# Kernel optimization log

Hardware: AMD Instinct MI355X
Metric: run time of the kernel (lower is better)

## Reference

```python
import jax, jax.numpy as jnp
from jax import lax
import numpy as np

N_NODES = 5000
N_EDGES = 80000
N_FEAT = 128
N_TPLT = 16
TPLT_NODES = 10
N_FW = 3         # Frank-Wolfe (conditional-gradient) outer iterations
SINK_ITERS = 10  # log-domain Sinkhorn inner iterations


def setup_inputs() -> dict:
    key = jax.random.key(0)
    k1, k2, k3, k4, k5 = jax.random.split(key, 5)
    x = jax.random.normal(k1, (N_NODES, N_FEAT), jnp.float32)
    src = jax.random.randint(k2, (N_EDGES,), 0, N_NODES, jnp.int32)
    dst = jax.random.randint(k3, (N_EDGES,), 0, N_NODES, jnp.int32)
    edge_index = jnp.stack([src, dst], axis=0)
    A0 = jax.random.uniform(k4, (N_TPLT, TPLT_NODES, TPLT_NODES), jnp.float32)
    tplt_adjacencies = 0.5 * (A0 + jnp.transpose(A0, (0, 2, 1)))  # symmetrized, as in template_initialisation
    tplt_features = jax.random.normal(k5, (N_TPLT, TPLT_NODES, N_FEAT), jnp.float32)
    q0 = jnp.zeros((N_TPLT, TPLT_NODES), jnp.float32)   # softmax(q0) -> uniform template node weights
    alpha0 = jnp.zeros((1,), jnp.float32)               # sigmoid(alpha0) -> alpha = 0.5
    return {"x": x, "edge_index": edge_index, "tplt_adjacencies": tplt_adjacencies,
            "tplt_features": tplt_features, "q0": q0, "alpha0": alpha0}


def _sinkhorn_log(G, logp, logq, reg):
    """Log-domain Sinkhorn solving min <G,T> + reg*KL(T | p q^T); returns T [N, m]."""
    def step(carry, _):
        f, g = carry
        f = reg * (logp - jax.scipy.special.logsumexp((g[None, :] - G) / reg, axis=1))
        g = reg * (logq - jax.scipy.special.logsumexp((f[:, None] - G) / reg, axis=0))
        return (f, g), None
    (f, g), _ = lax.scan(step, (jnp.zeros_like(logp), jnp.zeros_like(logq)), None, length=SINK_ITERS)
    return jnp.exp((f[:, None] + g[None, :] - G) / reg)


def _fgw_dist(A, x, p, C2, F2, q, alpha):
    """Fused Gromov-Wasserstein distance (square loss) between graph (A, x, p)
    and one template (C2, F2, q), solved by conditional gradient with Sinkhorn
    inner OT solves and exact quadratic line search."""
    # pairwise squared-euclidean feature cost M [N, m]
    M = jnp.sum(x * x, 1)[:, None] + jnp.sum(F2 * F2, 1)[None, :] - 2.0 * (x @ F2.T)
    # square-loss Gromov decomposition: L(C1,C2) (x) T = constC - 2 * C1 T C2
    constC = ((A * A) @ p)[:, None] + ((C2 * C2) @ q)[None, :]
    logp, logq = jnp.log(p), jnp.log(q)
    T0 = p[:, None] * q[None, :]

    def fw_step(T, _):
        ATC = A @ (T @ C2)                        # [N, m]
        tens = constC - 2.0 * ATC
        G = (1.0 - alpha) * M + 2.0 * alpha * tens  # linearized gradient
        reg = 0.05 * jnp.mean(jnp.abs(G)) + 1e-9
        Tn = _sinkhorn_log(G, logp, logq, reg)
        dT = Tn - T
        AdTC = A @ (dT @ C2)
        # cost(T + g*dT) = a g^2 + b g + c  (square-loss FGW)
        a = -2.0 * alpha * jnp.sum(AdTC * dT)
        b = (1.0 - alpha) * jnp.sum(M * dT) + alpha * (jnp.sum(constC * dT) - 4.0 * jnp.sum(ATC * dT))
        gamma = jnp.where(a > 0.0, jnp.clip(-b / (2.0 * a + 1e-16), 0.0, 1.0),
                          jnp.where(a + b < 0.0, 1.0, 0.0))
        return T + gamma * dT, None

    T, _ = lax.scan(fw_step, T0, None, length=N_FW)
    ATC = A @ (T @ C2)
    return (1.0 - alpha) * jnp.sum(M * T) + alpha * (jnp.sum(constC * T) - 2.0 * jnp.sum(ATC * T))


def reference(x, edge_index, tplt_adjacencies, tplt_features, q0, alpha0):
    N = x.shape[0]
    # dense adjacency from COO edge list (to_dense_adj equivalent)
    A = jnp.zeros((N, N), x.dtype).at[edge_index[0], edge_index[1]].set(1.0)
    p = jnp.full((N,), 1.0 / N, x.dtype)       # uniform graph node weights
    alpha = jax.nn.sigmoid(alpha0[0])          # trained FGW trade-off (multi_alpha=False)
    q = jax.nn.softmax(q0, axis=1)             # trained template node weights
    dists = jax.vmap(lambda C2, F2, qk: _fgw_dist(A, x, p, C2, F2, qk, alpha))(
        tplt_adjacencies, tplt_features, q)
    return dists  # [n_tplt] FGW-distance embedding of the graph
```

## Files before the change

kernel.cpp:

```cpp
#include <hip/hip_runtime.h>
#include <stdint.h>

typedef float    f32x4 __attribute__((ext_vector_type(4)));
typedef uint32_t u32x4 __attribute__((ext_vector_type(4)));

#define NN 5000
#define NE 80000
#define NF 128
#define NT 16
#define TN 10
#define NFW 3
#define NSK 10
#define PW (1.0f/5000.0f)
#define RB 128
#define GRX 40

#define OFF_DEG  0u
#define OFF_RP   20224u
#define OFF_CUR  40448u
#define OFF_COL  60672u
#define OFF_SC   380672u
#define SC_FLOATS 384
#define OFF_M    393216u
#define OFF_T    4233216u
#define OFF_G    8073216u
#define OFF_ATCM 11913216u
#define OFF_ATCT 13193216u
#define OFF_ADTM 13513216u
#define OFF_ADTT 14793216u
#define OFF_TNM  15113216u
#define OFF_TNT  16393216u
#define OFF_Y2M  16713216u
#define OFF_Y2T  17993216u

__device__ __forceinline__ uint32_t bfb(float x) {
  uint32_t u = __float_as_uint(x);
  return (u + 0x7fffu + ((u >> 16) & 1u)) >> 16;
}
__device__ __forceinline__ uint32_t pk(float a, float b) { return bfb(a) | (bfb(b) << 16); }
__device__ __forceinline__ float ubl(uint32_t u) { return __uint_as_float(u << 16); }
__device__ __forceinline__ float ubh(uint32_t u) { return __uint_as_float(u & 0xffff0000u); }
__device__ __forceinline__ float sigm(float z) { return 1.f / (1.f + __expf(-z)); }

__device__ __forceinline__ void ld12(const float* p, float* v) {
  f32x4 a = *(const f32x4*)p, b = *(const f32x4*)(p + 4), c = *(const f32x4*)(p + 8);
  v[0]=a[0]; v[1]=a[1]; v[2]=a[2]; v[3]=a[3]; v[4]=b[0]; v[5]=b[1]; v[6]=b[2]; v[7]=b[3];
  v[8]=c[0]; v[9]=c[1];
}
__device__ __forceinline__ void st12(float* p, const float* v) {
  *(f32x4*)p       = (f32x4){v[0], v[1], v[2], v[3]};
  *(f32x4*)(p + 4) = (f32x4){v[4], v[5], v[6], v[7]};
  *(f32x4*)(p + 8) = (f32x4){v[8], v[9], 0.f, 0.f};
}
__device__ __forceinline__ void ldbf(const u32x4* __restrict__ M4, const uint32_t* __restrict__ M1,
                                     size_t i, float* v) {
  u32x4 A = M4[i]; uint32_t B = M1[i];
  v[0]=ubl(A[0]); v[1]=ubh(A[0]); v[2]=ubl(A[1]); v[3]=ubh(A[1]);
  v[4]=ubl(A[2]); v[5]=ubh(A[2]); v[6]=ubl(A[3]); v[7]=ubh(A[3]);
  v[8]=ubl(B);    v[9]=ubh(B);
}
__device__ __forceinline__ void stbf(u32x4* __restrict__ M4, uint32_t* __restrict__ M1,
                                     size_t i, const float* v) {
  M4[i] = (u32x4){pk(v[0], v[1]), pk(v[2], v[3]), pk(v[4], v[5]), pk(v[6], v[7])};
  M1[i] = pk(v[8], v[9]);
}

__device__ __forceinline__ void gath(const u32x4* __restrict__ YM, const uint32_t* __restrict__ YT,
                                     const int* __restrict__ col, int e0, int e1, float* acc) {
  for (int e = e0; e < e1; ++e) {
    int c = col[e];
    u32x4 A = YM[c]; uint32_t B = YT[c];
    acc[0] += ubl(A[0]); acc[1] += ubh(A[0]); acc[2] += ubl(A[1]); acc[3] += ubh(A[1]);
    acc[4] += ubl(A[2]); acc[5] += ubh(A[2]); acc[6] += ubl(A[3]); acc[7] += ubh(A[3]);
    acc[8] += ubl(B);    acc[9] += ubh(B);
  }
}

__device__ __forceinline__ float get_gamma(const float* __restrict__ sc, int t, int k,
                                           float alpha, float oma) {
  const float* dk = sc + 64 + (size_t)((t - 1) * NT + k) * 4;
  float a_ = -2.f * alpha * dk[3];
  float b_ = oma * dk[0] + alpha * (dk[1] - 4.f * dk[2]);
  return (a_ > 0.f) ? fminf(fmaxf(-b_ / (2.f * a_ + 1e-16f), 0.f), 1.f)
                    : ((a_ + b_ < 0.f) ? 1.f : 0.f);
}

__global__ void k_init(char* __restrict__ ws) {
  int g = blockIdx.x * 256 + threadIdx.x;
  if (g < NN) ((int*)(ws + OFF_DEG))[g] = 0;
  int z = g - NN;
  if (z >= 0 && z < SC_FLOATS) ((float*)(ws + OFF_SC))[z] = 0.f;
}
__global__ void k_deg(const int* __restrict__ ei, int* __restrict__ deg) {
  int e = blockIdx.x * 256 + threadIdx.x;
  if (e < NE) atomicAdd(&deg[ei[e]], 1);
}
__global__ void k_scan(const int* __restrict__ deg, int* __restrict__ rowptr, int* __restrict__ cur) {
  __shared__ int scr[1024];
  int tid = threadIdx.x;
  int loc[5], s = 0;
  #pragma unroll
  for (int r = 0; r < 5; ++r) {
    int idx = tid * 5 + r;
    int d = (idx < NN) ? deg[idx] : 0;
    loc[r] = s; s += d;
  }
  scr[tid] = s; __syncthreads();
  for (int off = 1; off < 1024; off <<= 1) {
    int v = scr[tid];
    int u = (tid >= off) ? scr[tid - off] : 0;
    __syncthreads();
    scr[tid] = v + u;
    __syncthreads();
  }
  int base = (tid > 0) ? scr[tid - 1] : 0;
  #pragma unroll
  for (int r = 0; r < 5; ++r) {
    int idx = tid * 5 + r;
    if (idx < NN) { int v = base + loc[r]; rowptr[idx] = v; cur[idx] = v; }
  }
  if (tid == 1023) rowptr[NN] = scr[1023];
}
__global__ void k_fill(const int* __restrict__ ei, int* __restrict__ cur, int* __restrict__ col) {
  int e = blockIdx.x * 256 + threadIdx.x;
  if (e < NE) {
    int s = ei[e];
    int pos = atomicAdd(&cur[s], 1);
    col[pos] = ei[NE + e];
  }
}

__global__ void kM(const float* __restrict__ x, const float* __restrict__ F2,
                   float* __restrict__ Mb) {
  __shared__ float ffs[TN];
  const int k = blockIdx.y, tid = threadIdx.x;
  const int i = blockIdx.x * RB + tid;
  const float* Fk = F2 + (size_t)k * TN * NF;
  if (tid < TN) {
    float s = 0.f;
    for (int d = 0; d < NF; ++d) { float f = Fk[tid * NF + d]; s += f * f; }
    ffs[tid] = s;
  }
  __syncthreads();
  if (i >= NN) return;
  const f32x4* xr = (const f32x4*)(x + (size_t)i * NF);
  float acc[TN];
  #pragma unroll
  for (int j = 0; j < TN; ++j) acc[j] = 0.f;
  float xsq = 0.f;
  for (int dc = 0; dc < NF / 4; ++dc) {
    f32x4 xv = xr[dc];
    xsq += xv[0]*xv[0] + xv[1]*xv[1] + xv[2]*xv[2] + xv[3]*xv[3];
    #pragma unroll
    for (int j = 0; j < TN; ++j) {
      const float* Fj = Fk + j * NF + dc * 4;
      acc[j] += xv[0]*Fj[0] + xv[1]*Fj[1] + xv[2]*Fj[2] + xv[3]*Fj[3];
    }
  }
  float v[TN];
  #pragma unroll
  for (int j = 0; j < TN; ++j) v[j] = xsq + ffs[j] - 2.f * acc[j];
  st12(Mb + ((size_t)k * NN + i) * 12, v);
}

__global__ void kYG(const int* __restrict__ rowptr, const float* __restrict__ Mb,
                    float* __restrict__ Tb,
                    const u32x4* __restrict__ TnM, const uint32_t* __restrict__ TnT,
                    u32x4* __restrict__ AtM, uint32_t* __restrict__ AtT,
                    const u32x4* __restrict__ AdM, const uint32_t* __restrict__ AdT_,
                    float* __restrict__ Gb, const float* __restrict__ q0,
                    const float* __restrict__ C2g, const float* __restrict__ a0,
                    float* __restrict__ sc, int t) {
  __shared__ float qvs[16], c2qs[16], qC2s[16];
  __shared__ float redl[2];
  const int k = blockIdx.y, tid = threadIdx.x;
  const int i = blockIdx.x * RB + tid;
  const float* C2k = C2g + k * 100;
  if (tid < TN) {
    float mx = -1e30f, e[TN], s = 0.f;
    #pragma unroll
    for (int j = 0; j < TN; ++j) mx = fmaxf(mx, q0[k * TN + j]);
    #pragma unroll
    for (int j = 0; j < TN; ++j) { e[j] = __expf(q0[k * TN + j] - mx); s += e[j]; }
    float inv = 1.f / s;
    qvs[tid] = e[tid] * inv;
    float c2 = 0.f, qc = 0.f;
    #pragma unroll
    for (int l = 0; l < TN; ++l) {
      float c = C2k[tid * TN + l];
      c2 += c * c * e[l] * inv;
      qc += e[l] * inv * C2k[l * TN + tid];
    }
    c2qs[tid] = c2; qC2s[tid] = qc;
  }
  __syncthreads();
  const float alpha = sigm(a0[0]), oma = 1.f - alpha;
  float sabs = 0.f;
  if (i < NN) {
    const int deg = rowptr[i + 1] - rowptr[i];
    const float cc = (float)deg * PW;
    const size_t ro = ((size_t)k * NN + i) * 12;
    const size_t bi = (size_t)k * NN + i;
    float Trow[TN], Arow[TN];
    if (t == 0) {
      #pragma unroll
      for (int j = 0; j < TN; ++j) { Trow[j] = PW * qvs[j]; Arow[j] = (float)deg * PW * qC2s[j]; }
    } else {
      const float gamma = get_gamma(sc, t, k, alpha, oma);
      float tv[TN], nv[TN], av[TN], dv[TN];
      ld12(Tb + ro, tv);
      ldbf(TnM, TnT, bi, nv);
      ldbf(AtM, AtT, bi, av);
      ldbf(AdM, AdT_, bi, dv);
      #pragma unroll
      for (int j = 0; j < TN; ++j) {
        Trow[j] = tv[j] + gamma * (nv[j] - tv[j]);
        Arow[j] = av[j] + gamma * dv[j];
      }
    }
    st12(Tb + ro, Trow);
    stbf(AtM, AtT, bi, Arow);
    float mv[TN]; ld12(Mb + ro, mv);
    float Gv[TN];
    #pragma unroll
    for (int j = 0; j < TN; ++j) {
      float G = oma * mv[j] + 2.f * alpha * (cc + c2qs[j] - 2.f * Arow[j]);
      Gv[j] = G; sabs += fabsf(G);
    }
    st12(Gb + ro, Gv);
  }
  #pragma unroll
  for (int o = 32; o; o >>= 1) sabs += __shfl_xor(sabs, o, 64);
  if ((tid & 63) == 0) redl[tid >> 6] = sabs;
  __syncthreads();
  if (tid == 0) atomicAdd(sc + t * NT + k, redl[0] + redl[1]);
}

__global__ __launch_bounds__(1024) void kSink(const float* __restrict__ Gb,
                                              u32x4* __restrict__ TnM, uint32_t* __restrict__ TnT,
                                              const float* __restrict__ q0,
                                              const float* __restrict__ sc, int t) {
  __shared__ float red[16 * 16];
  __shared__ float wls[16];
  const int k = blockIdx.x, tid = threadIdx.x;
  const int wid = tid >> 6;
  float qme = 0.f;
  if (tid < TN) {
    float mx = -1e30f, e[TN], s = 0.f;
    #pragma unroll
    for (int j = 0; j < TN; ++j) mx = fmaxf(mx, q0[k * TN + j]);
    #pragma unroll
    for (int j = 0; j < TN; ++j) { e[j] = __expf(q0[k * TN + j] - mx); s += e[j]; }
    qme = e[tid] / s;
  }
  const float reg = 0.05f * sc[t * NT + k] * (1.f / (float)(NN * TN)) + 1e-9f;
  const float invreg = 1.f / reg;
  const float* Gk = Gb + (size_t)k * NN * 12;

  float E[5][TN];
  bool v[5];
  #pragma unroll
  for (int s = 0; s < 5; ++s) {
    int i = s * 1024 + tid;
    v[s] = i < NN;
    if (v[s]) ld12(Gk + (size_t)i * 12, E[s]);
  }
  #pragma unroll
  for (int s = 0; s < 5; ++s) {
    if (v[s]) {
      float mn = E[s][0];
      #pragma unroll
      for (int j = 1; j < TN; ++j) mn = fminf(mn, E[s][j]);
      #pragma unroll
      for (int j = 0; j < TN; ++j) E[s][j] = __expf(-(E[s][j] - mn) * invreg);
    } else {
      #pragma unroll
      for (int j = 0; j < TN; ++j) E[s][j] = 0.f;
    }
  }

  float wlr[TN], wpr[TN];
  #pragma unroll
  for (int j = 0; j < TN; ++j) { wlr[j] = 1.f; wpr[j] = 1.f; }
  for (int it = 0; it < NSK; ++it) {
    float csl[TN];
    #pragma unroll
    for (int j = 0; j < TN; ++j) csl[j] = 0.f;
    #pragma unroll
    for (int s = 0; s < 5; ++s) {
      float dot = 0.f;
      #pragma unroll
      for (int j = 0; j < TN; ++j) dot += E[s][j] * wlr[j];
      float u = PW * __builtin_amdgcn_rcpf(fmaxf(dot, 1e-35f));
      #pragma unroll
      for (int j = 0; j < TN; ++j) csl[j] += E[s][j] * u;
    }
    #pragma unroll
    for (int j = 0; j < TN; ++j) {
      float vv = csl[j];
      #pragma unroll
      for (int o = 32; o; o >>= 1) vv += __shfl_xor(vv, o, 64);
      if ((tid & 63) == j) red[wid * 16 + j] = vv;
    }
    __syncthreads();
    if (tid < TN) {
      float s = 0.f;
      #pragma unroll
      for (int w = 0; w < 16; ++w) s += red[w * 16 + tid];
      wls[tid] = qme * __builtin_amdgcn_rcpf(fmaxf(s, 1e-35f));
    }
    __syncthreads();
    #pragma unroll
    for (int j = 0; j < TN; ++j) { wpr[j] = wlr[j]; wlr[j] = wls[j]; }
  }
  u32x4* TM = TnM + (size_t)k * NN;
  uint32_t* TT = TnT + (size_t)k * NN;
  #pragma unroll
  for (int s = 0; s < 5; ++s) {
    if (v[s]) {
      int i = s * 1024 + tid;
      float dot = 0.f;
      #pragma unroll
      for (int j = 0; j < TN; ++j) dot += E[s][j] * wpr[j];
      float u = PW * __builtin_amdgcn_rcpf(fmaxf(dot, 1e-35f));
      float tn[TN];
      #pragma unroll
      for (int j = 0; j < TN; ++j) tn[j] = u * E[s][j] * wlr[j];
      stbf(TM, TT, (size_t)i, tn);
    }
  }
}

__global__ void kDT(const int* __restrict__ rowptr, const float* __restrict__ Mb,
                    const float* __restrict__ Tb,
                    const u32x4* __restrict__ TnM, const uint32_t* __restrict__ TnT,
                    const float* __restrict__ q0, const float* __restrict__ C2g,
                    u32x4* __restrict__ Y2M, uint32_t* __restrict__ Y2T,
                    float* __restrict__ sc, int t) {
  __shared__ float c2qs[16];
  __shared__ float redl[4];
  const int k = blockIdx.y, tid = threadIdx.x;
  const int i = blockIdx.x * RB + tid;
  const float* C2k = C2g + k * 100;
  if (tid < TN) {
    float mx = -1e30f, e[TN], s = 0.f;
    #pragma unroll
    for (int j = 0; j < TN; ++j) mx = fmaxf(mx, q0[k * TN + j]);
    #pragma unroll
    for (int j = 0; j < TN; ++j) { e[j] = __expf(q0[k * TN + j] - mx); s += e[j]; }
    float inv = 1.f / s, c2 = 0.f;
    #pragma unroll
    for (int l = 0; l < TN; ++l) { float c = C2k[tid * TN + l]; c2 += c * c * e[l] * inv; }
    c2qs[tid] = c2;
  }
  __syncthreads();
  float bM = 0.f, bC = 0.f;
  if (i < NN) {
    const size_t ro = ((size_t)k * NN + i) * 12;
    const size_t bi = (size_t)k * NN + i;
    float tv[TN], nv[TN], mv[TN], d[TN];
    ld12(Tb + ro, tv); ldbf(TnM, TnT, bi, nv); ld12(Mb + ro, mv);
    float cc = (float)(rowptr[i + 1] - rowptr[i]) * PW;
    #pragma unroll
    for (int j = 0; j < TN; ++j) {
      d[j] = nv[j] - tv[j];
      bM += mv[j] * d[j];
      bC += (cc + c2qs[j]) * d[j];
    }
    float y[TN];
    #pragma unroll
    for (int j = 0; j < TN; ++j) {
      float s = 0.f;
      #pragma unroll
      for (int l = 0; l < TN; ++l) s += d[l] * C2k[l * TN + j];
      y[j] = s;
    }
    stbf(Y2M + (size_t)k * NN, Y2T + (size_t)k * NN, (size_t)i, y);
  }
  #pragma unroll
  for (int o = 32; o; o >>= 1) { bM += __shfl_xor(bM, o, 64); bC += __shfl_xor(bC, o, 64); }
  if ((tid & 63) == 0) { int w = tid >> 6; redl[w * 2] = bM; redl[w * 2 + 1] = bC; }
  __syncthreads();
  if (tid == 0) {
    float* dk = sc + 64 + (size_t)(t * NT + k) * 4;
    atomicAdd(dk + 0, redl[0] + redl[2]);
    atomicAdd(dk + 1, redl[1] + redl[3]);
  }
}

__global__ void kA(const int* __restrict__ rowptr, const int* __restrict__ col,
                   const float* __restrict__ Tb,
                   const u32x4* __restrict__ TnM, const uint32_t* __restrict__ TnT,
                   const u32x4* __restrict__ AtM, const uint32_t* __restrict__ AtT,
                   const u32x4* __restrict__ Y2M, const uint32_t* __restrict__ Y2T,
                   u32x4* __restrict__ AdM, uint32_t* __restrict__ AdT_,
                   float* __restrict__ sc, int t) {
  __shared__ float redl[4];
  const int k = blockIdx.y, tid = threadIdx.x;
  const int i = blockIdx.x * RB + tid;
  float bA = 0.f, aacc = 0.f;
  if (i < NN) {
    const size_t ro = ((size_t)k * NN + i) * 12;
    const size_t bi = (size_t)k * NN + i;
    float tv[TN], nv[TN], av[TN];
    ld12(Tb + ro, tv); ldbf(TnM, TnT, bi, nv); ldbf(AtM, AtT, bi, av);
    int e0 = rowptr[i], e1 = rowptr[i + 1];
    float adt[TN];
    #pragma unroll
    for (int j = 0; j < TN; ++j) adt[j] = 0.f;
    gath(Y2M + (size_t)k * NN, Y2T + (size_t)k * NN, col, e0, e1, adt);
    #pragma unroll
    for (int j = 0; j < TN; ++j) {
      float d = nv[j] - tv[j];
      bA += av[j] * d;
      aacc += adt[j] * d;
    }
    stbf(AdM, AdT_, bi, adt);
  }
  #pragma unroll
  for (int o = 32; o; o >>= 1) { bA += __shfl_xor(bA, o, 64); aacc += __shfl_xor(aacc, o, 64); }
  if ((tid & 63) == 0) { int w = tid >> 6; redl[w * 2] = bA; redl[w * 2 + 1] = aacc; }
  __syncthreads();
  if (tid == 0) {
    float* dk = sc + 64 + (size_t)(t * NT + k) * 4;
    atomicAdd(dk + 2, redl[0] + redl[2]);
    atomicAdd(dk + 3, redl[1] + redl[3]);
  }
}

__global__ void kFinYG(const int* __restrict__ rowptr, const float* __restrict__ Mb,
                       const float* __restrict__ Tb,
                       const u32x4* __restrict__ TnM, const uint32_t* __restrict__ TnT,
                       const u32x4* __restrict__ AtM, const uint32_t* __restrict__ AtT,
                       const u32x4* __restrict__ AdM, const uint32_t* __restrict__ AdT_,
                       const float* __restrict__ q0, const float* __restrict__ C2g,
                       const float* __restrict__ a0, float* __restrict__ sc,
                       float* __restrict__ out) {
  __shared__ float c2qs[16];
  __shared__ float redl[6];
  const int k = blockIdx.y, tid = threadIdx.x;
  const int i = blockIdx.x * RB + tid;
  const float* C2k = C2g + k * 100;
  if (tid < TN) {
    float mx = -1e30f, e[TN], s = 0.f;
    #pragma unroll
    for (int j = 0; j < TN; ++j) mx = fmaxf(mx, q0[k * TN + j]);
    #pragma unroll
    for (int j = 0; j < TN; ++j) { e[j] = __expf(q0[k * TN + j] - mx); s += e[j]; }
    float inv = 1.f / s, c2 = 0.f;
    #pragma unroll
    for (int l = 0; l < TN; ++l) { float c = C2k[tid * TN + l]; c2 += c * c * e[l] * inv; }
    c2qs[tid] = c2;
  }
  __syncthreads();
  const float alpha = sigm(a0[0]), oma = 1.f - alpha;
  const float gamma = get_gamma(sc, NFW, k, alpha, oma);
  float d1 = 0.f, d2 = 0.f, d3 = 0.f;
  if (i < NN) {
    const size_t ro = ((size_t)k * NN + i) * 12;
    const size_t bi = (size_t)k * NN + i;
    float tv[TN], nv[TN], av[TN], dv[TN], mv[TN];
    ld12(Tb + ro, tv); ldbf(TnM, TnT, bi, nv);
    ldbf(AtM, AtT, bi, av); ldbf(AdM, AdT_, bi, dv);
    ld12(Mb + ro, mv);
    float cc = (float)(rowptr[i + 1] - rowptr[i]) * PW;
    #pragma unroll
    for (int j = 0; j < TN; ++j) {
      float Tf = tv[j] + gamma * (nv[j] - tv[j]);
      float Af = av[j] + gamma * dv[j];
      d1 += mv[j] * Tf;
      d2 += (cc + c2qs[j]) * Tf;
      d3 += Af * Tf;
    }
  }
  #pragma unroll
  for (int o = 32; o; o >>= 1) {
    d1 += __shfl_xor(d1, o, 64); d2 += __shfl_xor(d2, o, 64); d3 += __shfl_xor(d3, o, 64);
  }
  if ((tid & 63) == 0) {
    int w = tid >> 6;
    redl[w * 3] = d1; redl[w * 3 + 1] = d2; redl[w * 3 + 2] = d3;
  }
  __syncthreads();
  float* fk = sc + 256 + k * 4;
  if (tid == 0) {
    atomicAdd(fk + 0, redl[0] + redl[3]);
    atomicAdd(fk + 1, redl[1] + redl[4]);
    atomicAdd(fk + 2, redl[2] + redl[5]);
  }
  asm volatile("s_waitcnt vmcnt(0)" ::: "memory");
  __syncthreads();
  if (tid == 0) {
    int* ctr = (int*)sc + 320 + k;
    int old = __hip_atomic_fetch_add(ctr, 1, __ATOMIC_RELAXED, __HIP_MEMORY_SCOPE_AGENT);
    if (old == GRX - 1) {
      float f0 = __hip_atomic_fetch_add(fk + 0, 0.f, __ATOMIC_RELAXED, __HIP_MEMORY_SCOPE_AGENT);
      float f1 = __hip_atomic_fetch_add(fk + 1, 0.f, __ATOMIC_RELAXED, __HIP_MEMORY_SCOPE_AGENT);
      float f2 = __hip_atomic_fetch_add(fk + 2, 0.f, __ATOMIC_RELAXED, __HIP_MEMORY_SCOPE_AGENT);
      out[k] = oma * f0 + alpha * (f1 - 2.f * f2);
    }
  }
}

extern "C" void kernel_launch(void* const* d_in, const int* in_sizes, int n_in,
                              void* d_out, int out_size, void* d_ws, size_t ws_size,
                              hipStream_t stream) {
  const float* x  = (const float*)d_in[0];
  const int*   ei = (const int*)d_in[1];
  const float* C2 = (const float*)d_in[2];
  const float* F2 = (const float*)d_in[3];
  const float* q0 = (const float*)d_in[4];
  const float* a0 = (const float*)d_in[5];
  float* out = (float*)d_out;

  char* ws = (char*)d_ws;
  int* deg    = (int*)(ws + OFF_DEG);
  int* rowptr = (int*)(ws + OFF_RP);
  int* cur    = (int*)(ws + OFF_CUR);
  int* col    = (int*)(ws + OFF_COL);
  float* sc   = (float*)(ws + OFF_SC);
  float* Mb   = (float*)(ws + OFF_M);
  float* Tb   = (float*)(ws + OFF_T);
  float* Gb   = (float*)(ws + OFF_G);
  u32x4* AtM  = (u32x4*)(ws + OFF_ATCM);
  uint32_t* AtT = (uint32_t*)(ws + OFF_ATCT);
  u32x4* AdM  = (u32x4*)(ws + OFF_ADTM);
  uint32_t* AdT_ = (uint32_t*)(ws + OFF_ADTT);
  u32x4* TnM  = (u32x4*)(ws + OFF_TNM);
  uint32_t* TnT = (uint32_t*)(ws + OFF_TNT);
  u32x4* Y2M  = (u32x4*)(ws + OFF_Y2M);
  uint32_t* Y2T = (uint32_t*)(ws + OFF_Y2T);

  const dim3 rg(GRX, NT), rb(RB);

  k_init<<<(NN + SC_FLOATS + 255) / 256, 256, 0, stream>>>(ws);
  k_deg<<<(NE + 255) / 256, 256, 0, stream>>>(ei, deg);
  k_scan<<<1, 1024, 0, stream>>>(deg, rowptr, cur);
  k_fill<<<(NE + 255) / 256, 256, 0, stream>>>(ei, cur, col);
  kM<<<rg, rb, 0, stream>>>(x, F2, Mb);

  for (int t = 0; t < NFW; ++t) {
    kYG<<<rg, rb, 0, stream>>>(rowptr, Mb, Tb, TnM, TnT, AtM, AtT, AdM, AdT_,
                               Gb, q0, C2, a0, sc, t);
    kSink<<<NT, 1024, 0, stream>>>(Gb, TnM, TnT, q0, sc, t);
    kDT<<<rg, rb, 0, stream>>>(rowptr, Mb, Tb, TnM, TnT, q0, C2, Y2M, Y2T, sc, t);
    kA<<<rg, rb, 0, stream>>>(rowptr, col, Tb, TnM, TnT, AtM, AtT, Y2M, Y2T,
                              AdM, AdT_, sc, t);
  }
  kFinYG<<<rg, rb, 0, stream>>>(rowptr, Mb, Tb, TnM, TnT, AtM, AtT, AdM, AdT_,
                                q0, C2, a0, sc, out);
}
```

Before: 436.9 us.

## Fuse FW iteration kernels into cooperative per-template kernel with group barriers

Replaces the four per-iteration kernels (gradient, Sinkhorn, direction, adjacency product) with one cooperative kernel per Frank-Wolfe step. Each template is handled by 16 blocks that keep their rows' T, A·T·C2, cost and Gibbs kernel in registers, and Sinkhorn column sums are exchanged through global atomics and spin barriers. The line-search update is folded into the start of the next launch, so the G buffer and the Tn buffer are no longer written or read. This cuts kernel launch count and round-trips through global memory. In exchange it adds ten spin barriers per iteration over global atomics, and its correctness depends on all 256 blocks being co-resident.

```diff
diff --git a/kernel.cpp b/kernel.cpp
--- a/kernel.cpp
+++ b/kernel.cpp
@@ -14,24 +14,26 @@
 #define PW (1.0f/5000.0f)
 #define RB 128
 #define GRX 40
+#define NBT 16
+#define TPB 320
+#define RPB 313
 
 #define OFF_DEG  0u
 #define OFF_RP   20224u
 #define OFF_CUR  40448u
 #define OFF_COL  60672u
 #define OFF_SC   380672u
+#define OFF_CS   382208u
+#define OFF_M    416000u
+#define OFF_T    4256000u
+#define OFF_ATM  8096000u
+#define OFF_ATT  9376000u
+#define OFF_DTM  9696000u
+#define OFF_DTT  10976000u
+#define OFF_Y2M  11296000u
+#define OFF_Y2T  12576000u
 #define SC_FLOATS 384
-#define OFF_M    393216u
-#define OFF_T    4233216u
-#define OFF_G    8073216u
-#define OFF_ATCM 11913216u
-#define OFF_ATCT 13193216u
-#define OFF_ADTM 13513216u
-#define OFF_ADTT 14793216u
-#define OFF_TNM  15113216u
-#define OFF_TNT  16393216u
-#define OFF_Y2M  16713216u
-#define OFF_Y2T  17993216u
+#define CS_FLOATS 7680
 
 __device__ __forceinline__ uint32_t bfb(float x) {
   uint32_t u = __float_as_uint(x);
@@ -64,7 +66,6 @@
   M4[i] = (u32x4){pk(v[0], v[1]), pk(v[2], v[3]), pk(v[4], v[5]), pk(v[6], v[7])};
   M1[i] = pk(v[8], v[9]);
 }
-
 __device__ __forceinline__ void gath(const u32x4* __restrict__ YM, const uint32_t* __restrict__ YT,
                                      const int* __restrict__ col, int e0, int e1, float* acc) {
   for (int e = e0; e < e1; ++e) {
@@ -75,14 +76,26 @@
     acc[8] += ubl(B);    acc[9] += ubh(B);
   }
 }
-
-__device__ __forceinline__ float get_gamma(const float* __restrict__ sc, int t, int k,
-                                           float alpha, float oma) {
-  const float* dk = sc + 64 + (size_t)((t - 1) * NT + k) * 4;
-  float a_ = -2.f * alpha * dk[3];
-  float b_ = oma * dk[0] + alpha * (dk[1] - 4.f * dk[2]);
-  return (a_ > 0.f) ? fminf(fmaxf(-b_ / (2.f * a_ + 1e-16f), 0.f), 1.f)
-                    : ((a_ + b_ < 0.f) ? 1.f : 0.f);
+__device__ __forceinline__ float ga_readf(float* p) {
+  return __hip_atomic_fetch_add(p, 0.0f, __ATOMIC_RELAXED, __HIP_MEMORY_SCOPE_AGENT);
+}
+__device__ __forceinline__ void tbar(int* ctr, int target) {
+  asm volatile("s_waitcnt vmcnt(0)" ::: "memory");
+  __syncthreads();
+  if (threadIdx.x == 0) {
+    __hip_atomic_fetch_add(ctr, 1, __ATOMIC_RELAXED, __HIP_MEMORY_SCOPE_AGENT);
+    while (__hip_atomic_fetch_add(ctr, 0, __ATOMIC_RELAXED, __HIP_MEMORY_SCOPE_AGENT) < target)
+      __builtin_amdgcn_s_sleep(8);
+  }
+  __syncthreads();
+}
+__device__ __forceinline__ float bred(float v, float* red) {
+  #pragma unroll
+  for (int o = 32; o; o >>= 1) v += __shfl_xor(v, o, 64);
+  __syncthreads();
+  if ((threadIdx.x & 63) == 0) red[threadIdx.x >> 6] = v;
+  __syncthreads();
+  return red[0] + red[1] + red[2] + red[3] + red[4];
 }
 
 __global__ void k_init(char* __restrict__ ws) {
@@ -90,6 +103,8 @@
   if (g < NN) ((int*)(ws + OFF_DEG))[g] = 0;
   int z = g - NN;
   if (z >= 0 && z < SC_FLOATS) ((float*)(ws + OFF_SC))[z] = 0.f;
+  int c = g - (NN + SC_FLOATS);
+  if (c >= 0 && c < CS_FLOATS) ((float*)(ws + OFF_CS))[c] = 0.f;
 }
 __global__ void k_deg(const int* __restrict__ ei, int* __restrict__ deg) {
   int e = blockIdx.x * 256 + threadIdx.x;
@@ -129,7 +144,6 @@
     col[pos] = ei[NE + e];
   }
 }
-
 __global__ void kM(const float* __restrict__ x, const float* __restrict__ F2,
                    float* __restrict__ Mb) {
   __shared__ float ffs[TN];
@@ -163,18 +177,21 @@
   st12(Mb + ((size_t)k * NN + i) * 12, v);
 }
 
-__global__ void kYG(const int* __restrict__ rowptr, const float* __restrict__ Mb,
-                    float* __restrict__ Tb,
-                    const u32x4* __restrict__ TnM, const uint32_t* __restrict__ TnT,
-                    u32x4* __restrict__ AtM, uint32_t* __restrict__ AtT,
-                    const u32x4* __restrict__ AdM, const uint32_t* __restrict__ AdT_,
-                    float* __restrict__ Gb, const float* __restrict__ q0,
-                    const float* __restrict__ C2g, const float* __restrict__ a0,
-                    float* __restrict__ sc, int t) {
+__global__ __launch_bounds__(TPB, 2) void kFW(
+    const int* __restrict__ rowptr, const int* __restrict__ col,
+    const float* __restrict__ Mb, float* __restrict__ Tb,
+    u32x4* __restrict__ AtM, uint32_t* __restrict__ AtT,
+    u32x4* __restrict__ DtM, uint32_t* __restrict__ DtT,
+    u32x4* __restrict__ Y2M, uint32_t* __restrict__ Y2T,
+    const float* __restrict__ q0, const float* __restrict__ C2g,
+    const float* __restrict__ a0p, float* __restrict__ sc,
+    float* __restrict__ csg, int t) {
+  __shared__ float red[80];
+  __shared__ float csb[16];
   __shared__ float qvs[16], c2qs[16], qC2s[16];
-  __shared__ float redl[2];
-  const int k = blockIdx.y, tid = threadIdx.x;
-  const int i = blockIdx.x * RB + tid;
+  const int bid = blockIdx.x;
+  const int k = bid >> 4, b = bid & (NBT - 1);
+  const int tid = threadIdx.x;
   const float* C2k = C2g + k * 100;
   if (tid < TN) {
     float mx = -1e30f, e[TN], s = 0.f;
@@ -194,153 +211,157 @@
     c2qs[tid] = c2; qC2s[tid] = qc;
   }
   __syncthreads();
-  const float alpha = sigm(a0[0]), oma = 1.f - alpha;
+  const float alpha = sigm(a0p[0]), oma = 1.f - alpha;
+  int* ctr = (int*)sc + 320 + t * 16 + k;
+  int barno = 0;
+
+  const int r = b * RPB + tid;
+  const bool own = (tid < RPB) && (r < NN);
+  int e0 = 0, e1 = 0;
+  if (own) { e0 = rowptr[r]; e1 = rowptr[r + 1]; }
+  const float cc = (float)(e1 - e0) * PW;
+  const size_t bi = (size_t)k * NN + (own ? r : 0);
+
+  float Tr[TN], Ar[TN];
+  if (t == 0) {
+    if (own) {
+      #pragma unroll
+      for (int j = 0; j < TN; ++j) { Tr[j] = PW * qvs[j]; Ar[j] = (float)(e1 - e0) * PW * qC2s[j]; }
+    }
+  } else {
+    float adt[TN] = {0,0,0,0,0,0,0,0,0,0};
+    float av[TN], dv[TN];
+    float bA = 0.f, aA = 0.f;
+    if (own) {
+      gath(Y2M + (size_t)k * NN, Y2T + (size_t)k * NN, col, e0, e1, adt);
+      ldbf(AtM, AtT, bi, av); ldbf(DtM, DtT, bi, dv);
+      #pragma unroll
+      for (int j = 0; j < TN; ++j) { bA += av[j] * dv[j]; aA += adt[j] * dv[j]; }
+    }
+    bA = bred(bA, red); aA = bred(aA, red);
+    float* dk = sc + 64 + (size_t)((t - 1) * NT + k) * 4;
+    if (tid == 0) { atomicAdd(dk + 2, bA); atomicAdd(dk + 3, aA); }
+    tbar(ctr, ++barno * NBT);
+    if (tid < 4) csb[tid] = ga_readf(dk + tid);
+    __syncthreads();
+    float a_ = -2.f * alpha * csb[3];
+    float b_ = oma * csb[0] + alpha * (csb[1] - 4.f * csb[2]);
+    float gamma = (a_ > 0.f) ? fminf(fmaxf(-b_ / (2.f * a_ + 1e-16f), 0.f), 1.f)
+                             : ((a_ + b_ < 0.f) ? 1.f : 0.f);
+    if (own) {
+      float tv[TN]; ld12(Tb + bi * 12, tv);
+      #pragma unroll
+      for (int j = 0; j < TN; ++j) { Tr[j] = tv[j] + gamma * dv[j]; Ar[j] = av[j] + gamma * adt[j]; }
+    }
+  }
+  float Mr[TN], Er[TN];
   float sabs = 0.f;
-  if (i < NN) {
-    const int deg = rowptr[i + 1] - rowptr[i];
-    const float cc = (float)deg * PW;
-    const size_t ro = ((size_t)k * NN + i) * 12;
-    const size_t bi = (size_t)k * NN + i;
-    float Trow[TN], Arow[TN];
-    if (t == 0) {
-      #pragma unroll
-      for (int j = 0; j < TN; ++j) { Trow[j] = PW * qvs[j]; Arow[j] = (float)deg * PW * qC2s[j]; }
-    } else {
-      const float gamma = get_gamma(sc, t, k, alpha, oma);
-      float tv[TN], nv[TN], av[TN], dv[TN];
-      ld12(Tb + ro, tv);
-      ldbf(TnM, TnT, bi, nv);
-      ldbf(AtM, AtT, bi, av);
-      ldbf(AdM, AdT_, bi, dv);
-      #pragma unroll
-      for (int j = 0; j < TN; ++j) {
-        Trow[j] = tv[j] + gamma * (nv[j] - tv[j]);
-        Arow[j] = av[j] + gamma * dv[j];
-      }
-    }
-    st12(Tb + ro, Trow);
-    stbf(AtM, AtT, bi, Arow);
-    float mv[TN]; ld12(Mb + ro, mv);
-    float Gv[TN];
-    #pragma unroll
-    for (int j = 0; j < TN; ++j) {
-      float G = oma * mv[j] + 2.f * alpha * (cc + c2qs[j] - 2.f * Arow[j]);
-      Gv[j] = G; sabs += fabsf(G);
-    }
-    st12(Gb + ro, Gv);
-  }
-  #pragma unroll
-  for (int o = 32; o; o >>= 1) sabs += __shfl_xor(sabs, o, 64);
-  if ((tid & 63) == 0) redl[tid >> 6] = sabs;
-  __syncthreads();
-  if (tid == 0) atomicAdd(sc + t * NT + k, redl[0] + redl[1]);
-}
-
-__global__ __launch_bounds__(1024) void kSink(const float* __restrict__ Gb,
-                                              u32x4* __restrict__ TnM, uint32_t* __restrict__ TnT,
-                                              const float* __restrict__ q0,
-                                              const float* __restrict__ sc, int t) {
-  __shared__ float red[16 * 16];
-  __shared__ float wls[16];
-  const int k = blockIdx.x, tid = threadIdx.x;
-  const int wid = tid >> 6;
-  float qme = 0.f;
-  if (tid < TN) {
-    float mx = -1e30f, e[TN], s = 0.f;
-    #pragma unroll
-    for (int j = 0; j < TN; ++j) mx = fmaxf(mx, q0[k * TN + j]);
-    #pragma unroll
-    for (int j = 0; j < TN; ++j) { e[j] = __expf(q0[k * TN + j] - mx); s += e[j]; }
-    qme = e[tid] / s;
-  }
-  const float reg = 0.05f * sc[t * NT + k] * (1.f / (float)(NN * TN)) + 1e-9f;
-  const float invreg = 1.f / reg;
-  const float* Gk = Gb + (size_t)k * NN * 12;
-
-  float E[5][TN];
-  bool v[5];
-  #pragma unroll
-  for (int s = 0; s < 5; ++s) {
-    int i = s * 1024 + tid;
-    v[s] = i < NN;
-    if (v[s]) ld12(Gk + (size_t)i * 12, E[s]);
-  }
-  #pragma unroll
-  for (int s = 0; s < 5; ++s) {
-    if (v[s]) {
-      float mn = E[s][0];
-      #pragma unroll
-      for (int j = 1; j < TN; ++j) mn = fminf(mn, E[s][j]);
-      #pragma unroll
-      for (int j = 0; j < TN; ++j) E[s][j] = __expf(-(E[s][j] - mn) * invreg);
-    } else {
-      #pragma unroll
-      for (int j = 0; j < TN; ++j) E[s][j] = 0.f;
-    }
+  if (own) {
+    st12(Tb + bi * 12, Tr);
+    stbf(AtM, AtT, bi, Ar);
+    ld12(Mb + bi * 12, Mr);
+    #pragma unroll
+    for (int j = 0; j < TN; ++j) {
+      float G = oma * Mr[j] + 2.f * alpha * (cc + c2qs[j] - 2.f * Ar[j]);
+      Er[j] = G; sabs += fabsf(G);
+    }
+  }
+  sabs = bred(sabs, red);
+  if (tid == 0) atomicAdd(sc + t * NT + k, sabs);
+  tbar(ctr, ++barno * NBT);
+  if (tid == 0) csb[0] = ga_readf(sc + t * NT + k);
+  __syncthreads();
+  const float invreg = 1.f / (0.05f * csb[0] * (1.f / (float)(NN * TN)) + 1e-9f);
+  if (own) {
+    float mn = Er[0];
+    #pragma unroll
+    for (int j = 1; j < TN; ++j) mn = fminf(mn, Er[j]);
+    #pragma unroll
+    for (int j = 0; j < TN; ++j) Er[j] = __expf(-(Er[j] - mn) * invreg);
+  } else {
+    #pragma unroll
+    for (int j = 0; j < TN; ++j) Er[j] = 0.f;
   }
 
   float wlr[TN], wpr[TN];
   #pragma unroll
   for (int j = 0; j < TN; ++j) { wlr[j] = 1.f; wpr[j] = 1.f; }
   for (int it = 0; it < NSK; ++it) {
+    float dot = 0.f;
+    #pragma unroll
+    for (int j = 0; j < TN; ++j) dot += Er[j] * wlr[j];
+    float u = PW * __builtin_amdgcn_rcpf(fmaxf(dot, 1e-35f));
     float csl[TN];
     #pragma unroll
-    for (int j = 0; j < TN; ++j) csl[j] = 0.f;
-    #pragma unroll
-    for (int s = 0; s < 5; ++s) {
-      float dot = 0.f;
-      #pragma unroll
-      for (int j = 0; j < TN; ++j) dot += E[s][j] * wlr[j];
-      float u = PW * __builtin_amdgcn_rcpf(fmaxf(dot, 1e-35f));
-      #pragma unroll
-      for (int j = 0; j < TN; ++j) csl[j] += E[s][j] * u;
-    }
+    for (int j = 0; j < TN; ++j) csl[j] = Er[j] * u;
     #pragma unroll
     for (int j = 0; j < TN; ++j) {
       float vv = csl[j];
       #pragma unroll
       for (int o = 32; o; o >>= 1) vv += __shfl_xor(vv, o, 64);
-      if ((tid & 63) == j) red[wid * 16 + j] = vv;
+      if ((tid & 63) == j) red[(tid >> 6) * 16 + j] = vv;
     }
     __syncthreads();
+    float* cell = csg + (size_t)((t * NSK + it) * NT + k) * 16;
     if (tid < TN) {
+      float s = red[tid] + red[16 + tid] + red[32 + tid] + red[48 + tid] + red[64 + tid];
+      atomicAdd(cell + tid, s);
+    }
+    tbar(ctr, ++barno * NBT);
+    if (tid < TN) csb[tid] = ga_readf(cell + tid);
+    __syncthreads();
+    #pragma unroll
+    for (int j = 0; j < TN; ++j) {
+      wpr[j] = wlr[j];
+      wlr[j] = qvs[j] * __builtin_amdgcn_rcpf(fmaxf(csb[j], 1e-35f));
+    }
+  }
+
+  float bM = 0.f, bC = 0.f;
+  if (own) {
+    float dot = 0.f;
+    #pragma unroll
+    for (int j = 0; j < TN; ++j) dot += Er[j] * wpr[j];
+    float u = PW * __builtin_amdgcn_rcpf(fmaxf(dot, 1e-35f));
+    float dT[TN];
+    #pragma unroll
+    for (int j = 0; j < TN; ++j) {
+      float tn = u * Er[j] * wlr[j];
+      dT[j] = tn - Tr[j];
+      bM += Mr[j] * dT[j];
+      bC += (cc + c2qs[j]) * dT[j];
+    }
+    stbf(DtM, DtT, bi, dT);
+    float y[TN];
+    #pragma unroll
+    for (int j = 0; j < TN; ++j) {
       float s = 0.f;
       #pragma unroll
-      for (int w = 0; w < 16; ++w) s += red[w * 16 + tid];
-      wls[tid] = qme * __builtin_amdgcn_rcpf(fmaxf(s, 1e-35f));
-    }
-    __syncthreads();
-    #pragma unroll
-    for (int j = 0; j < TN; ++j) { wpr[j] = wlr[j]; wlr[j] = wls[j]; }
-  }
-  u32x4* TM = TnM + (size_t)k * NN;
-  uint32_t* TT = TnT + (size_t)k * NN;
-  #pragma unroll
-  for (int s = 0; s < 5; ++s) {
-    if (v[s]) {
-      int i = s * 1024 + tid;
-      float dot = 0.f;
-      #pragma unroll
-      for (int j = 0; j < TN; ++j) dot += E[s][j] * wpr[j];
-      float u = PW * __builtin_amdgcn_rcpf(fmaxf(dot, 1e-35f));
-      float tn[TN];
-      #pragma unroll
-      for (int j = 0; j < TN; ++j) tn[j] = u * E[s][j] * wlr[j];
-      stbf(TM, TT, (size_t)i, tn);
-    }
-  }
-}
-
-__global__ void kDT(const int* __restrict__ rowptr, const float* __restrict__ Mb,
-                    const float* __restrict__ Tb,
-                    const u32x4* __restrict__ TnM, const uint32_t* __restrict__ TnT,
-                    const float* __restrict__ q0, const float* __restrict__ C2g,
-                    u32x4* __restrict__ Y2M, uint32_t* __restrict__ Y2T,
-                    float* __restrict__ sc, int t) {
+      for (int l = 0; l < TN; ++l) s += dT[l] * C2k[l * TN + j];
+      y[j] = s;
+    }
+    stbf(Y2M, Y2T, bi, y);
+  }
+  bM = bred(bM, red); bC = bred(bC, red);
+  float* dk2 = sc + 64 + (size_t)(t * NT + k) * 4;
+  if (tid == 0) { atomicAdd(dk2 + 0, bM); atomicAdd(dk2 + 1, bC); }
+}
+
+__global__ __launch_bounds__(TPB, 2) void kFin(
+    const int* __restrict__ rowptr, const int* __restrict__ col,
+    const float* __restrict__ Mb, const float* __restrict__ Tb,
+    const u32x4* __restrict__ AtM, const uint32_t* __restrict__ AtT,
+    const u32x4* __restrict__ DtM, const uint32_t* __restrict__ DtT,
+    const u32x4* __restrict__ Y2M, const uint32_t* __restrict__ Y2T,
+    const float* __restrict__ q0, const float* __restrict__ C2g,
+    const float* __restrict__ a0p, float* __restrict__ sc,
+    float* __restrict__ out) {
+  __shared__ float red[80];
+  __shared__ float csb[16];
   __shared__ float c2qs[16];
-  __shared__ float redl[4];
-  const int k = blockIdx.y, tid = threadIdx.x;
-  const int i = blockIdx.x * RB + tid;
+  const int bid = blockIdx.x;
+  const int k = bid >> 4, b = bid & (NBT - 1);
+  const int tid = threadIdx.x;
   const float* C2k = C2g + k * 100;
   if (tid < TN) {
     float mx = -1e30f, e[TN], s = 0.f;
@@ -354,152 +375,53 @@
     c2qs[tid] = c2;
   }
   __syncthreads();
-  float bM = 0.f, bC = 0.f;
-  if (i < NN) {
-    const size_t ro = ((size_t)k * NN + i) * 12;
-    const size_t bi = (size_t)k * NN + i;
-    float tv[TN], nv[TN], mv[TN], d[TN];
-    ld12(Tb + ro, tv); ldbf(TnM, TnT, bi, nv); ld12(Mb + ro, mv);
-    float cc = (float)(rowptr[i + 1] - rowptr[i]) * PW;
-    #pragma unroll
-    for (int j = 0; j < TN; ++j) {
-      d[j] = nv[j] - tv[j];
-      bM += mv[j] * d[j];
-      bC += (cc + c2qs[j]) * d[j];
-    }
-    float y[TN];
-    #pragma unroll
-    for (int j = 0; j < TN; ++j) {
-      float s = 0.f;
-      #pragma unroll
-      for (int l = 0; l < TN; ++l) s += d[l] * C2k[l * TN + j];
-      y[j] = s;
-    }
-    stbf(Y2M + (size_t)k * NN, Y2T + (size_t)k * NN, (size_t)i, y);
-  }
-  #pragma unroll
-  for (int o = 32; o; o >>= 1) { bM += __shfl_xor(bM, o, 64); bC += __shfl_xor(bC, o, 64); }
-  if ((tid & 63) == 0) { int w = tid >> 6; redl[w * 2] = bM; redl[w * 2 + 1] = bC; }
-  __syncthreads();
-  if (tid == 0) {
-    float* dk = sc + 64 + (size_t)(t * NT + k) * 4;
-    atomicAdd(dk + 0, redl[0] + redl[2]);
-    atomicAdd(dk + 1, redl[1] + redl[3]);
-  }
-}
-
-__global__ void kA(const int* __restrict__ rowptr, const int* __restrict__ col,
-                   const float* __restrict__ Tb,
-                   const u32x4* __restrict__ TnM, const uint32_t* __restrict__ TnT,
-                   const u32x4* __restrict__ AtM, const uint32_t* __restrict__ AtT,
-                   const u32x4* __restrict__ Y2M, const uint32_t* __restrict__ Y2T,
-                   u32x4* __restrict__ AdM, uint32_t* __restrict__ AdT_,
-                   float* __restrict__ sc, int t) {
-  __shared__ float redl[4];
-  const int k = blockIdx.y, tid = threadIdx.x;
-  const int i = blockIdx.x * RB + tid;
-  float bA = 0.f, aacc = 0.f;
-  if (i < NN) {
-    const size_t ro = ((size_t)k * NN + i) * 12;
-    const size_t bi = (size_t)k * NN + i;
-    float tv[TN], nv[TN], av[TN];
-    ld12(Tb + ro, tv); ldbf(TnM, TnT, bi, nv); ldbf(AtM, AtT, bi, av);
-    int e0 = rowptr[i], e1 = rowptr[i + 1];
-    float adt[TN];
-    #pragma unroll
-    for (int j = 0; j < TN; ++j) adt[j] = 0.f;
+  const float alpha = sigm(a0p[0]), oma = 1.f - alpha;
+  int* ctr = (int*)sc + 320 + 3 * 16 + k;
+  const int r = b * RPB + tid;
+  const bool own = (tid < RPB) && (r < NN);
+  int e0 = 0, e1 = 0;
+  if (own) { e0 = rowptr[r]; e1 = rowptr[r + 1]; }
+  const float cc = (float)(e1 - e0) * PW;
+  const size_t bi = (size_t)k * NN + (own ? r : 0);
+
+  float adt[TN] = {0,0,0,0,0,0,0,0,0,0};
+  float av[TN], dv[TN];
+  float bA = 0.f, aA = 0.f;
+  if (own) {
     gath(Y2M + (size_t)k * NN, Y2T + (size_t)k * NN, col, e0, e1, adt);
-    #pragma unroll
-    for (int j = 0; j < TN; ++j) {
-      float d = nv[j] - tv[j];
-      bA += av[j] * d;
-      aacc += adt[j] * d;
-    }
-    stbf(AdM, AdT_, bi, adt);
-  }
-  #pragma unroll
-  for (int o = 32; o; o >>= 1) { bA += __shfl_xor(bA, o, 64); aacc += __shfl_xor(aacc, o, 64); }
-  if ((tid & 63) == 0) { int w = tid >> 6; redl[w * 2] = bA; redl[w * 2 + 1] = aacc; }
-  __syncthreads();
-  if (tid == 0) {
-    float* dk = sc + 64 + (size_t)(t * NT + k) * 4;
-    atomicAdd(dk + 2, redl[0] + redl[2]);
-    atomicAdd(dk + 3, redl[1] + redl[3]);
-  }
-}
-
-__global__ void kFinYG(const int* __restrict__ rowptr, const float* __restrict__ Mb,
-                       const float* __restrict__ Tb,
-                       const u32x4* __restrict__ TnM, const uint32_t* __restrict__ TnT,
-                       const u32x4* __restrict__ AtM, const uint32_t* __restrict__ AtT,
-                       const u32x4* __restrict__ AdM, const uint32_t* __restrict__ AdT_,
-                       const float* __restrict__ q0, const float* __restrict__ C2g,
-                       const float* __restrict__ a0, float* __restrict__ sc,
-                       float* __restrict__ out) {
-  __shared__ float c2qs[16];
-  __shared__ float redl[6];
-  const int k = blockIdx.y, tid = threadIdx.x;
-  const int i = blockIdx.x * RB + tid;
-  const float* C2k = C2g + k * 100;
-  if (tid < TN) {
-    float mx = -1e30f, e[TN], s = 0.f;
-    #pragma unroll
-    for (int j = 0; j < TN; ++j) mx = fmaxf(mx, q0[k * TN + j]);
-    #pragma unroll
-    for (int j = 0; j < TN; ++j) { e[j] = __expf(q0[k * TN + j] - mx); s += e[j]; }
-    float inv = 1.f / s, c2 = 0.f;
-    #pragma unroll
-    for (int l = 0; l < TN; ++l) { float c = C2k[tid * TN + l]; c2 += c * c * e[l] * inv; }
-    c2qs[tid] = c2;
-  }
-  __syncthreads();
-  const float alpha = sigm(a0[0]), oma = 1.f - alpha;
-  const float gamma = get_gamma(sc, NFW, k, alpha, oma);
+    ldbf(AtM, AtT, bi, av); ldbf(DtM, DtT, bi, dv);
+    #pragma unroll
+    for (int j = 0; j < TN; ++j) { bA += av[j] * dv[j]; aA += adt[j] * dv[j]; }
+  }
+  bA = bred(bA, red); aA = bred(aA, red);
+  float* dk = sc + 64 + (size_t)((NFW - 1) * NT + k) * 4;
+  if (tid == 0) { atomicAdd(dk + 2, bA); atomicAdd(dk + 3, aA); }
+  tbar(ctr, 1 * NBT);
+  if (tid < 4) csb[tid] = ga_readf(dk + tid);
+  __syncthreads();
+  float a_ = -2.f * alpha * csb[3];
+  float b_ = oma * csb[0] + alpha * (csb[1] - 4.f * csb[2]);
+  float gamma = (a_ > 0.f) ? fminf(fmaxf(-b_ / (2.f * a_ + 1e-16f), 0.f), 1.f)
+                           : ((a_ + b_ < 0.f) ? 1.f : 0.f);
   float d1 = 0.f, d2 = 0.f, d3 = 0.f;
-  if (i < NN) {
-    const size_t ro = ((size_t)k * NN + i) * 12;
-    const size_t bi = (size_t)k * NN + i;
-    float tv[TN], nv[TN], av[TN], dv[TN], mv[TN];
-    ld12(Tb + ro, tv); ldbf(TnM, TnT, bi, nv);
-    ldbf(AtM, AtT, bi, av); ldbf(AdM, AdT_, bi, dv);
-    ld12(Mb + ro, mv);
-    float cc = (float)(rowptr[i + 1] - rowptr[i]) * PW;
-    #pragma unroll
-    for (int j = 0; j < TN; ++j) {
-      float Tf = tv[j] + gamma * (nv[j] - tv[j]);
-      float Af = av[j] + gamma * dv[j];
+  if (own) {
+    float tv[TN], mv[TN];
+    ld12(Tb + bi * 12, tv); ld12(Mb + bi * 12, mv);
+    #pragma unroll
+    for (int j = 0; j < TN; ++j) {
+      float Tf = tv[j] + gamma * dv[j];
+      float Af = av[j] + gamma * adt[j];
       d1 += mv[j] * Tf;
       d2 += (cc + c2qs[j]) * Tf;
       d3 += Af * Tf;
     }
   }
-  #pragma unroll
-  for (int o = 32; o; o >>= 1) {
-    d1 += __shfl_xor(d1, o, 64); d2 += __shfl_xor(d2, o, 64); d3 += __shfl_xor(d3, o, 64);
-  }
-  if ((tid & 63) == 0) {
-    int w = tid >> 6;
-    redl[w * 3] = d1; redl[w * 3 + 1] = d2; redl[w * 3 + 2] = d3;
-  }
-  __syncthreads();
+  d1 = bred(d1, red); d2 = bred(d2, red); d3 = bred(d3, red);
   float* fk = sc + 256 + k * 4;
-  if (tid == 0) {
-    atomicAdd(fk + 0, redl[0] + redl[3]);
-    atomicAdd(fk + 1, redl[1] + redl[4]);
-    atomicAdd(fk + 2, redl[2] + redl[5]);
-  }
-  asm volatile("s_waitcnt vmcnt(0)" ::: "memory");
-  __syncthreads();
-  if (tid == 0) {
-    int* ctr = (int*)sc + 320 + k;
-    int old = __hip_atomic_fetch_add(ctr, 1, __ATOMIC_RELAXED, __HIP_MEMORY_SCOPE_AGENT);
-    if (old == GRX - 1) {
-      float f0 = __hip_atomic_fetch_add(fk + 0, 0.f, __ATOMIC_RELAXED, __HIP_MEMORY_SCOPE_AGENT);
-      float f1 = __hip_atomic_fetch_add(fk + 1, 0.f, __ATOMIC_RELAXED, __HIP_MEMORY_SCOPE_AGENT);
-      float f2 = __hip_atomic_fetch_add(fk + 2, 0.f, __ATOMIC_RELAXED, __HIP_MEMORY_SCOPE_AGENT);
-      out[k] = oma * f0 + alpha * (f1 - 2.f * f2);
-    }
-  }
+  if (tid == 0) { atomicAdd(fk + 0, d1); atomicAdd(fk + 1, d2); atomicAdd(fk + 2, d3); }
+  tbar(ctr, 2 * NBT);
+  if (b == 0 && tid == 0)
+    out[k] = oma * ga_readf(fk + 0) + alpha * (ga_readf(fk + 1) - 2.f * ga_readf(fk + 2));
 }
 
 extern "C" void kernel_launch(void* const* d_in, const int* in_sizes, int n_in,
@@ -510,7 +432,7 @@
   const float* C2 = (const float*)d_in[2];
   const float* F2 = (const float*)d_in[3];
   const float* q0 = (const float*)d_in[4];
-  const float* a0 = (const float*)d_in[5];
+  const float* a0p = (const float*)d_in[5];
   float* out = (float*)d_out;
 
   char* ws = (char*)d_ws;
@@ -519,34 +441,36 @@
   int* cur    = (int*)(ws + OFF_CUR);
   int* col    = (int*)(ws + OFF_COL);
   float* sc   = (float*)(ws + OFF_SC);
+  float* csg  = (float*)(ws + OFF_CS);
   float* Mb   = (float*)(ws + OFF_M);
   float* Tb   = (float*)(ws + OFF_T);
-  float* Gb   = (float*)(ws + OFF_G);
-  u32x4* AtM  = (u32x4*)(ws + OFF_ATCM);
-  uint32_t* AtT = (uint32_t*)(ws + OFF_ATCT);
-  u32x4* AdM  = (u32x4*)(ws + OFF_ADTM);
-  uint32_t* AdT_ = (uint32_t*)(ws + OFF_ADTT);
-  u32x4* TnM  = (u32x4*)(ws + OFF_TNM);
-  uint32_t* TnT = (uint32_t*)(ws + OFF_TNT);
+  u32x4* AtM  = (u32x4*)(ws + OFF_ATM);
+  uint32_t* AtT = (uint32_t*)(ws + OFF_ATT);
+  u32x4* DtM  = (u32x4*)(ws + OFF_DTM);
+  uint32_t* DtT = (uint32_t*)(ws + OFF_DTT);
   u32x4* Y2M  = (u32x4*)(ws + OFF_Y2M);
   uint32_t* Y2T = (uint32_t*)(ws + OFF_Y2T);
 
-  const dim3 rg(GRX, NT), rb(RB);
-
-  k_init<<<(NN + SC_FLOATS + 255) / 256, 256, 0, stream>>>(ws);
+  int initN = NN + SC_FLOATS + CS_FLOATS;
+  k_init<<<(initN + 255) / 256, 256, 0, stream>>>(ws);
   k_deg<<<(NE + 255) / 256, 256, 0, stream>>>(ei, deg);
   k_scan<<<1, 1024, 0, stream>>>(deg, rowptr, cur);
   k_fill<<<(NE + 255) / 256, 256, 0, stream>>>(ei, cur, col);
-  kM<<<rg, rb, 0, stream>>>(x, F2, Mb);
-
+  kM<<<dim3(GRX, NT), RB, 0, stream>>>(x, F2, Mb);
+
+  int tv[NFW] = {0, 1, 2};
   for (int t = 0; t < NFW; ++t) {
-    kYG<<<rg, rb, 0, stream>>>(rowptr, Mb, Tb, TnM, TnT, AtM, AtT, AdM, AdT_,
-                               Gb, q0, C2, a0, sc, t);
-    kSink<<<NT, 1024, 0, stream>>>(Gb, TnM, TnT, q0, sc, t);
-    kDT<<<rg, rb, 0, stream>>>(rowptr, Mb, Tb, TnM, TnT, q0, C2, Y2M, Y2T, sc, t);
-    kA<<<rg, rb, 0, stream>>>(rowptr, col, Tb, TnM, TnT, AtM, AtT, Y2M, Y2T,
-                              AdM, AdT_, sc, t);
-  }
-  kFinYG<<<rg, rb, 0, stream>>>(rowptr, Mb, Tb, TnM, TnT, AtM, AtT, AdM, AdT_,
-                                q0, C2, a0, sc, out);
-}
+    void* args[] = { (void*)&rowptr, (void*)&col, (void*)&Mb, (void*)&Tb,
+                     (void*)&AtM, (void*)&AtT, (void*)&DtM, (void*)&DtT,
+                     (void*)&Y2M, (void*)&Y2T, (void*)&q0, (void*)&C2,
+                     (void*)&a0p, (void*)&sc, (void*)&csg, (void*)&tv[t] };
+    hipLaunchCooperativeKernel((const void*)kFW, dim3(NT * NBT), dim3(TPB),
+                               args, 0, stream);
+  }
+  void* fargs[] = { (void*)&rowptr, (void*)&col, (void*)&Mb, (void*)&Tb,
+                    (void*)&AtM, (void*)&AtT, (void*)&DtM, (void*)&DtT,
+                    (void*)&Y2M, (void*)&Y2T, (void*)&q0, (void*)&C2,
+                    (void*)&a0p, (void*)&sc, (void*)&out };
+  hipLaunchCooperativeKernel((const void*)kFin, dim3(NT * NBT), dim3(TPB),
+                             fargs, 0, stream);
+}
```

Result: slower. 598.9 us (+37.1%).
